# Optimization experiments

Hardware: AMD Instinct MI355X
Metric: run time of the kernel (lower is better)

Reference implementation:

```python
import jax, jax.numpy as jnp
import numpy as np
import math

DIM, NH, NKV, HD = 4096, 32, 8, 128
BLOCK, NBLK, TOPK = 256, 128, 16


def apply_rope(x, cos, sin):
    # x: [b, l, h, d]; cos/sin: [l, d//2] -- complex multiply on (even, odd) pairs
    b, l, h, d = x.shape
    xr = x.reshape(b, l, h, d // 2, 2)
    xe, xo = xr[..., 0], xr[..., 1]
    c = cos[None, :, None, :]
    s = sin[None, :, None, :]
    oe = xe * c - xo * s
    oo = xe * s + xo * c
    return jnp.stack([oe, oo], axis=-1).reshape(b, l, h, d)


def setup_inputs() -> dict:
    key = jax.random.key(0)
    ks = jax.random.split(key, 8)
    x = jax.random.normal(ks[0], (1, 1, DIM), dtype=jnp.float32)
    # real RoPE angles for position start_pos (llama3 theta=500000)
    start_pos = 4096
    inv_freq = 1.0 / (500000.0 ** (np.arange(0, HD, 2, dtype=np.float32) / HD))
    ang = np.float32(start_pos) * inv_freq  # [HD//2]
    freqs_cos = jnp.asarray(np.cos(ang))[None, :]  # [1, 64]
    freqs_sin = jnp.asarray(np.sin(ang))[None, :]
    sc = 0.02
    wq = jax.random.normal(ks[1], (NH * HD, DIM), dtype=jnp.float32) * sc
    wk = jax.random.normal(ks[2], (NKV * HD, DIM), dtype=jnp.float32) * sc
    wv = jax.random.normal(ks[3], (NKV * HD, DIM), dtype=jnp.float32) * sc
    wo = jax.random.normal(ks[4], (DIM, NH * HD), dtype=jnp.float32) * sc
    k_cache = jax.random.normal(ks[5], (NBLK, BLOCK, NKV, HD), dtype=jnp.float32)
    v_cache = jax.random.normal(ks[6], (NBLK, BLOCK, NKV, HD), dtype=jnp.float32)
    block_idx = jnp.sort(jax.random.randint(ks[7], (TOPK,), 0, NBLK, dtype=jnp.int32))
    return {"x": x, "freqs_cos": freqs_cos, "freqs_sin": freqs_sin,
            "wq": wq, "wk": wk, "wv": wv, "wo": wo,
            "k_cache": k_cache, "v_cache": v_cache, "block_idx": block_idx}


def reference(x, freqs_cos, freqs_sin, wq, wk, wv, wo, k_cache, v_cache, block_idx):
    b, l, _ = x.shape
    n_rep = NH // NKV
    # QKV projections (torch Linear: y = x @ W.T)
    q = (x @ wq.T).reshape(b, l, NH, HD)
    k = (x @ wk.T).reshape(b, l, NKV, HD)
    v = (x @ wv.T).reshape(b, l, NKV, HD)
    q = apply_rope(q, freqs_cos, freqs_sin)
    k = apply_rope(k, freqs_cos, freqs_sin)
    # fetch selected top-k blocks from KV cache: [K, BLOCK, NKV, HD] -> [K*BLOCK, NKV, HD]
    k_sel = k_cache[block_idx].reshape(-1, NKV, HD)
    v_sel = v_cache[block_idx].reshape(-1, NKV, HD)
    # append current step's k/v (offloader.push of the current block)
    k_full = jnp.concatenate([k_sel, k[0]], axis=0)  # [T, NKV, HD]
    v_full = jnp.concatenate([v_sel, v[0]], axis=0)
    # -> [1, NKV, T, HD], GQA repeat_interleave over head dim -> [1, NH, T, HD]
    k_full = jnp.repeat(k_full.transpose(1, 0, 2)[None], n_rep, axis=1)
    v_full = jnp.repeat(v_full.transpose(1, 0, 2)[None], n_rep, axis=1)
    qh = q.transpose(0, 2, 1, 3)  # [b, NH, l, HD]
    scores = jnp.einsum('bhld,bhtd->bhlt', qh, k_full) / math.sqrt(HD)
    attn = jax.nn.softmax(scores, axis=-1)
    out = jnp.einsum('bhlt,bhtd->bhld', attn, v_full)
    out = out.transpose(0, 2, 1, 3).reshape(b, l, NH * HD)
    return out @ wo.T
```

## Files before the change

kernel.cpp:

```cpp
#include <hip/hip_runtime.h>
#include <math.h>

#define DIM   4096
#define NH    32
#define NKV   8
#define HD    128
#define KVBLK 256
#define TOPK  16
#define SCALE 0.08838834764831845f

#define WS_Q   0
#define WS_K   4096
#define WS_V   5120
#define WS_M   6144
#define WS_L   7168
#define WS_O   8192
#define WS_AO  139264

__global__ __launch_bounds__(256) void qkv_rope_kernel(
    const float* __restrict__ x,
    const float* __restrict__ wq,
    const float* __restrict__ wk,
    const float* __restrict__ wv,
    const float* __restrict__ cvec,
    const float* __restrict__ svec,
    float* __restrict__ ws)
{
  const int tid  = threadIdx.x;
  const int wave = tid >> 6;
  const int lane = tid & 63;
  const int base = blockIdx.x * 4;
  const int row  = base + wave;

  const float* W;
  int r;
  if (row < 4096)      { W = wq; r = row; }
  else if (row < 5120) { W = wk; r = row - 4096; }
  else                 { W = wv; r = row - 5120; }

  const float4* w4 = (const float4*)(W + (size_t)r * DIM);
  const float4* x4 = (const float4*)x;

  float acc = 0.f;
#pragma unroll
  for (int i = 0; i < 16; ++i) {
    float4 a = x4[lane + i * 64];
    float4 b = w4[lane + i * 64];
    acc += a.x * b.x + a.y * b.y + a.z * b.z + a.w * b.w;
  }
#pragma unroll
  for (int off = 32; off > 0; off >>= 1)
    acc += __shfl_xor(acc, off, 64);

  __shared__ float sval[4];
  if (lane == 0) sval[wave] = acc;
  __syncthreads();

  if (tid < 2) {
    const int pr    = tid;
    const int row_e = base + 2 * pr;
    const float xe = sval[2 * pr];
    const float xo = sval[2 * pr + 1];
    if (row_e < 5120) {
      const int j   = (row_e & (HD - 1)) >> 1;
      const float c = cvec[j], s = svec[j];
      const float oe = xe * c - xo * s;
      const float oo = xe * s + xo * c;
      if (row_e < 4096) {
        ws[WS_Q + row_e]     = oe;
        ws[WS_Q + row_e + 1] = oo;
      } else {
        ws[WS_K + row_e - 4096] = oe;
        ws[WS_K + row_e - 4095] = oo;
      }
    } else {
      ws[WS_V + row_e - 5120] = xe;
      ws[WS_V + row_e - 5119] = xo;
    }
  }
}

__global__ __launch_bounds__(256) void attn_partial_kernel(
    const float* __restrict__ kc,
    const float* __restrict__ vc,
    const int*   __restrict__ bidx,
    float* __restrict__ ws)
{
  const int chunk = blockIdx.x;
  const int kvh   = blockIdx.y;
  const int tid   = threadIdx.x;
  const int wave  = tid >> 6;
  const int lane  = tid & 63;

  __shared__ float4 kv4[128 * 32];

  const int cb      = bidx[chunk >> 1];
  const int posbase = (chunk & 1) * 128;
  const size_t basef4 = ((((size_t)cb * KVBLK + posbase) * NKV + kvh) * HD) / 4;
  const float4* ksrc = (const float4*)kc + basef4;
  const float4* vsrc = (const float4*)vc + basef4;

#pragma unroll
  for (int i = 0; i < 16; ++i) {
    const int idx = tid + i * 256;
    const int p   = idx >> 5;
    const int d4  = idx & 31;
    kv4[p * 32 + (d4 ^ (p & 31))] = ksrc[(size_t)p * 256 + d4];
  }
  __syncthreads();

  const int qh = kvh * 4 + wave;
  const float4* qg4 = (const float4*)(ws + WS_Q + (size_t)qh * HD);

  float s0 = 0.f, s1 = 0.f;
  const int p0 = lane, p1 = lane + 64;
#pragma unroll
  for (int d4 = 0; d4 < 32; ++d4) {
    const float4 qv = qg4[d4];
    const float4 k0 = kv4[p0 * 32 + (d4 ^ (p0 & 31))];
    const float4 k1 = kv4[p1 * 32 + (d4 ^ (p1 & 31))];
    s0 += qv.x * k0.x + qv.y * k0.y + qv.z * k0.z + qv.w * k0.w;
    s1 += qv.x * k1.x + qv.y * k1.y + qv.z * k1.z + qv.w * k1.w;
  }
  s0 *= SCALE; s1 *= SCALE;

  float m = fmaxf(s0, s1);
#pragma unroll
  for (int off = 32; off > 0; off >>= 1)
    m = fmaxf(m, __shfl_xor(m, off, 64));
  const float e0 = __expf(s0 - m);
  const float e1 = __expf(s1 - m);
  float l = e0 + e1;
#pragma unroll
  for (int off = 32; off > 0; off >>= 1)
    l += __shfl_xor(l, off, 64);

  __syncthreads();
#pragma unroll
  for (int i = 0; i < 16; ++i) {
    const int idx = tid + i * 256;
    const int p   = idx >> 5;
    const int d4  = idx & 31;
    kv4[p * 32 + d4] = vsrc[(size_t)p * 256 + d4];
  }
  __syncthreads();

  float2 o = make_float2(0.f, 0.f);
  const float2* v2 = (const float2*)kv4;
#pragma unroll 8
  for (int t = 0; t < 128; ++t) {
    const float e = (t < 64) ? __shfl(e0, t, 64) : __shfl(e1, t - 64, 64);
    const float2 vv = v2[(size_t)t * 64 + lane];
    o.x += e * vv.x;
    o.y += e * vv.y;
  }

  const int pc = qh * 32 + chunk;
  if (lane == 0) {
    ws[WS_M + pc] = m;
    ws[WS_L + pc] = l;
  }
  ((float2*)(ws + WS_O + (size_t)pc * HD))[lane] = o;
}

__global__ __launch_bounds__(128) void attn_reduce_kernel(float* __restrict__ ws)
{
  const int qh  = blockIdx.x;
  const int d   = threadIdx.x;
  const int kvh = qh >> 2;

  __shared__ float red[128];
  red[d] = ws[WS_Q + qh * HD + d] * ws[WS_K + kvh * HD + d];
  __syncthreads();
  for (int off = 64; off > 0; off >>= 1) {
    if (d < off) red[d] += red[d + off];
    __syncthreads();
  }
  const float s_new = red[0] * SCALE;

  float m_g = s_new;
  for (int c = 0; c < 32; ++c)
    m_g = fmaxf(m_g, ws[WS_M + qh * 32 + c]);

  const float w_new = __expf(s_new - m_g);
  float l_g = w_new;
  float o_d = w_new * ws[WS_V + kvh * HD + d];
  for (int c = 0; c < 32; ++c) {
    const float mc = ws[WS_M + qh * 32 + c];
    const float lc = ws[WS_L + qh * 32 + c];
    const float w  = __expf(mc - m_g);
    l_g += lc * w;
    o_d += w * ws[WS_O + (size_t)(qh * 32 + c) * HD + d];
  }
  ws[WS_AO + qh * HD + d] = o_d / l_g;
}

__global__ __launch_bounds__(256) void oproj_kernel(
    const float* __restrict__ wo,
    const float* __restrict__ ws,
    float* __restrict__ out)
{
  const int tid  = threadIdx.x;
  const int wave = tid >> 6;
  const int lane = tid & 63;
  const int row  = blockIdx.x * 4 + wave;

  const float4* w4 = (const float4*)(wo + (size_t)row * DIM);
  const float4* a4 = (const float4*)(ws + WS_AO);

  float acc = 0.f;
#pragma unroll
  for (int i = 0; i < 16; ++i) {
    float4 a = a4[lane + i * 64];
    float4 b = w4[lane + i * 64];
    acc += a.x * b.x + a.y * b.y + a.z * b.z + a.w * b.w;
  }
#pragma unroll
  for (int off = 32; off > 0; off >>= 1)
    acc += __shfl_xor(acc, off, 64);

  if (lane == 0) out[row] = acc;
}

extern "C" void kernel_launch(void* const* d_in, const int* in_sizes, int n_in,
                              void* d_out, int out_size, void* d_ws, size_t ws_size,
                              hipStream_t stream)
{
  const float* x    = (const float*)d_in[0];
  const float* fcos = (const float*)d_in[1];
  const float* fsin = (const float*)d_in[2];
  const float* wq   = (const float*)d_in[3];
  const float* wk   = (const float*)d_in[4];
  const float* wv   = (const float*)d_in[5];
  const float* wo   = (const float*)d_in[6];
  const float* kc   = (const float*)d_in[7];
  const float* vc   = (const float*)d_in[8];
  const int*   bidx = (const int*)d_in[9];
  float* out = (float*)d_out;
  float* ws  = (float*)d_ws;

  qkv_rope_kernel<<<1536, 256, 0, stream>>>(x, wq, wk, wv, fcos, fsin, ws);
  attn_partial_kernel<<<dim3(32, 8), 256, 0, stream>>>(kc, vc, bidx, ws);
  attn_reduce_kernel<<<32, 128, 0, stream>>>(ws);
  oproj_kernel<<<1024, 256, 0, stream>>>(wo, ws, out);
}
```

Baseline: 346.2 us.

## Compute two rows per wave in GEMVs and split attention into 64-token chunks

The QKV and output-projection GEMV kernels now have each wave compute two adjacent rows. QKV computes each RoPE pair in one wave, which removes the shared-memory exchange and the barrier, and both kernels launch half as many blocks. The attention partial kernel splits KV into 64-token chunks (64 per kv head) and loads K and V into separate shared buffers up front, so the V load no longer waits on the QK step. This doubles the partial grid and the reduce work, and the workspace layout changes to fit the extra partials.

```diff
diff --git a/kernel.cpp b/kernel.cpp
--- a/kernel.cpp
+++ b/kernel.cpp
@@ -7,15 +7,16 @@
 #define HD    128
 #define KVBLK 256
 #define TOPK  16
+#define NCHUNK 64
 #define SCALE 0.08838834764831845f
 
 #define WS_Q   0
 #define WS_K   4096
 #define WS_V   5120
 #define WS_M   6144
-#define WS_L   7168
-#define WS_O   8192
-#define WS_AO  139264
+#define WS_L   8192
+#define WS_O   10240
+#define WS_AO  272384
 
 __global__ __launch_bounds__(256) void qkv_rope_kernel(
     const float* __restrict__ x,
@@ -29,38 +30,36 @@
   const int tid  = threadIdx.x;
   const int wave = tid >> 6;
   const int lane = tid & 63;
-  const int base = blockIdx.x * 4;
-  const int row  = base + wave;
+  const int pair = blockIdx.x * 4 + wave;
+  const int row_e = pair * 2;
 
   const float* W;
   int r;
-  if (row < 4096)      { W = wq; r = row; }
-  else if (row < 5120) { W = wk; r = row - 4096; }
-  else                 { W = wv; r = row - 5120; }
-
-  const float4* w4 = (const float4*)(W + (size_t)r * DIM);
-  const float4* x4 = (const float4*)x;
-
-  float acc = 0.f;
-#pragma unroll
+  if (row_e < 4096)      { W = wq; r = row_e; }
+  else if (row_e < 5120) { W = wk; r = row_e - 4096; }
+  else                   { W = wv; r = row_e - 5120; }
+
+  const float4* we4 = (const float4*)(W + (size_t)r * DIM);
+  const float4* wo4 = (const float4*)(W + (size_t)(r + 1) * DIM);
+  const float4* x4  = (const float4*)x;
+
+  float acc_e = 0.f, acc_o = 0.f;
+#pragma unroll 8
   for (int i = 0; i < 16; ++i) {
-    float4 a = x4[lane + i * 64];
-    float4 b = w4[lane + i * 64];
-    acc += a.x * b.x + a.y * b.y + a.z * b.z + a.w * b.w;
-  }
-#pragma unroll
-  for (int off = 32; off > 0; off >>= 1)
-    acc += __shfl_xor(acc, off, 64);
-
-  __shared__ float sval[4];
-  if (lane == 0) sval[wave] = acc;
-  __syncthreads();
-
-  if (tid < 2) {
-    const int pr    = tid;
-    const int row_e = base + 2 * pr;
-    const float xe = sval[2 * pr];
-    const float xo = sval[2 * pr + 1];
+    const float4 a  = x4[lane + i * 64];
+    const float4 be = we4[lane + i * 64];
+    const float4 bo = wo4[lane + i * 64];
+    acc_e += a.x * be.x + a.y * be.y + a.z * be.z + a.w * be.w;
+    acc_o += a.x * bo.x + a.y * bo.y + a.z * bo.z + a.w * bo.w;
+  }
+#pragma unroll
+  for (int off = 32; off > 0; off >>= 1) {
+    acc_e += __shfl_xor(acc_e, off, 64);
+    acc_o += __shfl_xor(acc_o, off, 64);
+  }
+
+  if (lane == 0) {
+    const float xe = acc_e, xo = acc_o;
     if (row_e < 5120) {
       const int j   = (row_e & (HD - 1)) >> 1;
       const float c = cvec[j], s = svec[j];
@@ -92,70 +91,65 @@
   const int wave  = tid >> 6;
   const int lane  = tid & 63;
 
-  __shared__ float4 kv4[128 * 32];
-
-  const int cb      = bidx[chunk >> 1];
-  const int posbase = (chunk & 1) * 128;
+  __shared__ float4 k4[64 * 32];
+  __shared__ float4 v4s[64 * 32];
+
+  const int cb      = bidx[chunk >> 2];
+  const int posbase = (chunk & 3) * 64;
   const size_t basef4 = ((((size_t)cb * KVBLK + posbase) * NKV + kvh) * HD) / 4;
   const float4* ksrc = (const float4*)kc + basef4;
   const float4* vsrc = (const float4*)vc + basef4;
 
 #pragma unroll
-  for (int i = 0; i < 16; ++i) {
+  for (int i = 0; i < 8; ++i) {
     const int idx = tid + i * 256;
     const int p   = idx >> 5;
     const int d4  = idx & 31;
-    kv4[p * 32 + (d4 ^ (p & 31))] = ksrc[(size_t)p * 256 + d4];
+    k4[p * 32 + (d4 ^ (p & 31))] = ksrc[(size_t)p * 256 + d4];
+  }
+#pragma unroll
+  for (int i = 0; i < 8; ++i) {
+    const int idx = tid + i * 256;
+    const int p   = idx >> 5;
+    const int d4  = idx & 31;
+    v4s[p * 32 + d4] = vsrc[(size_t)p * 256 + d4];
   }
   __syncthreads();
 
   const int qh = kvh * 4 + wave;
   const float4* qg4 = (const float4*)(ws + WS_Q + (size_t)qh * HD);
 
-  float s0 = 0.f, s1 = 0.f;
-  const int p0 = lane, p1 = lane + 64;
+  float s0 = 0.f;
+  const int p0 = lane;
 #pragma unroll
   for (int d4 = 0; d4 < 32; ++d4) {
     const float4 qv = qg4[d4];
-    const float4 k0 = kv4[p0 * 32 + (d4 ^ (p0 & 31))];
-    const float4 k1 = kv4[p1 * 32 + (d4 ^ (p1 & 31))];
+    const float4 k0 = k4[p0 * 32 + (d4 ^ (p0 & 31))];
     s0 += qv.x * k0.x + qv.y * k0.y + qv.z * k0.z + qv.w * k0.w;
-    s1 += qv.x * k1.x + qv.y * k1.y + qv.z * k1.z + qv.w * k1.w;
-  }
-  s0 *= SCALE; s1 *= SCALE;
-
-  float m = fmaxf(s0, s1);
+  }
+  s0 *= SCALE;
+
+  float m = s0;
 #pragma unroll
   for (int off = 32; off > 0; off >>= 1)
     m = fmaxf(m, __shfl_xor(m, off, 64));
   const float e0 = __expf(s0 - m);
-  const float e1 = __expf(s1 - m);
-  float l = e0 + e1;
+  float l = e0;
 #pragma unroll
   for (int off = 32; off > 0; off >>= 1)
     l += __shfl_xor(l, off, 64);
 
-  __syncthreads();
-#pragma unroll
-  for (int i = 0; i < 16; ++i) {
-    const int idx = tid + i * 256;
-    const int p   = idx >> 5;
-    const int d4  = idx & 31;
-    kv4[p * 32 + d4] = vsrc[(size_t)p * 256 + d4];
-  }
-  __syncthreads();
-
   float2 o = make_float2(0.f, 0.f);
-  const float2* v2 = (const float2*)kv4;
+  const float2* v2 = (const float2*)v4s;
 #pragma unroll 8
-  for (int t = 0; t < 128; ++t) {
-    const float e = (t < 64) ? __shfl(e0, t, 64) : __shfl(e1, t - 64, 64);
+  for (int t = 0; t < 64; ++t) {
+    const float e = __shfl(e0, t, 64);
     const float2 vv = v2[(size_t)t * 64 + lane];
     o.x += e * vv.x;
     o.y += e * vv.y;
   }
 
-  const int pc = qh * 32 + chunk;
+  const int pc = qh * NCHUNK + chunk;
   if (lane == 0) {
     ws[WS_M + pc] = m;
     ws[WS_L + pc] = l;
@@ -179,18 +173,18 @@
   const float s_new = red[0] * SCALE;
 
   float m_g = s_new;
-  for (int c = 0; c < 32; ++c)
-    m_g = fmaxf(m_g, ws[WS_M + qh * 32 + c]);
+  for (int c = 0; c < NCHUNK; ++c)
+    m_g = fmaxf(m_g, ws[WS_M + qh * NCHUNK + c]);
 
   const float w_new = __expf(s_new - m_g);
   float l_g = w_new;
   float o_d = w_new * ws[WS_V + kvh * HD + d];
-  for (int c = 0; c < 32; ++c) {
-    const float mc = ws[WS_M + qh * 32 + c];
-    const float lc = ws[WS_L + qh * 32 + c];
+  for (int c = 0; c < NCHUNK; ++c) {
+    const float mc = ws[WS_M + qh * NCHUNK + c];
+    const float lc = ws[WS_L + qh * NCHUNK + c];
     const float w  = __expf(mc - m_g);
     l_g += lc * w;
-    o_d += w * ws[WS_O + (size_t)(qh * 32 + c) * HD + d];
+    o_d += w * ws[WS_O + (size_t)(qh * NCHUNK + c) * HD + d];
   }
   ws[WS_AO + qh * HD + d] = o_d / l_g;
 }
@@ -203,23 +197,32 @@
   const int tid  = threadIdx.x;
   const int wave = tid >> 6;
   const int lane = tid & 63;
-  const int row  = blockIdx.x * 4 + wave;
-
-  const float4* w4 = (const float4*)(wo + (size_t)row * DIM);
-  const float4* a4 = (const float4*)(ws + WS_AO);
-
-  float acc = 0.f;
-#pragma unroll
+  const int pair = blockIdx.x * 4 + wave;
+  const int r0   = pair * 2;
+
+  const float4* w04 = (const float4*)(wo + (size_t)r0 * DIM);
+  const float4* w14 = (const float4*)(wo + (size_t)(r0 + 1) * DIM);
+  const float4* a4  = (const float4*)(ws + WS_AO);
+
+  float acc0 = 0.f, acc1 = 0.f;
+#pragma unroll 8
   for (int i = 0; i < 16; ++i) {
-    float4 a = a4[lane + i * 64];
-    float4 b = w4[lane + i * 64];
-    acc += a.x * b.x + a.y * b.y + a.z * b.z + a.w * b.w;
-  }
-#pragma unroll
-  for (int off = 32; off > 0; off >>= 1)
-    acc += __shfl_xor(acc, off, 64);
-
-  if (lane == 0) out[row] = acc;
+    const float4 a  = a4[lane + i * 64];
+    const float4 b0 = w04[lane + i * 64];
+    const float4 b1 = w14[lane + i * 64];
+    acc0 += a.x * b0.x + a.y * b0.y + a.z * b0.z + a.w * b0.w;
+    acc1 += a.x * b1.x + a.y * b1.y + a.z * b1.z + a.w * b1.w;
+  }
+#pragma unroll
+  for (int off = 32; off > 0; off >>= 1) {
+    acc0 += __shfl_xor(acc0, off, 64);
+    acc1 += __shfl_xor(acc1, off, 64);
+  }
+
+  if (lane == 0) {
+    out[r0]     = acc0;
+    out[r0 + 1] = acc1;
+  }
 }
 
 extern "C" void kernel_launch(void* const* d_in, const int* in_sizes, int n_in,
@@ -239,8 +242,8 @@
   float* out = (float*)d_out;
   float* ws  = (float*)d_ws;
 
-  qkv_rope_kernel<<<1536, 256, 0, stream>>>(x, wq, wk, wv, fcos, fsin, ws);
-  attn_partial_kernel<<<dim3(32, 8), 256, 0, stream>>>(kc, vc, bidx, ws);
+  qkv_rope_kernel<<<768, 256, 0, stream>>>(x, wq, wk, wv, fcos, fsin, ws);
+  attn_partial_kernel<<<dim3(NCHUNK, NKV), 256, 0, stream>>>(kc, vc, bidx, ws);
   attn_reduce_kernel<<<32, 128, 0, stream>>>(ws);
-  oproj_kernel<<<1024, 256, 0, stream>>>(wo, ws, out);
-}
+  oproj_kernel<<<512, 256, 0, stream>>>(wo, ws, out);
+}
```

After: 352.2 us. Within noise of the previous version (+1.7%).
